# Performance work log

Hardware: AMD Instinct MI355X
Metric: run time of the kernel (lower is better)

## Reference

```python
import jax, jax.numpy as jnp
import numpy as np

N_HEADS = 16
EPS = 1e-6

def _feature_map(x):
    return jax.nn.elu(x) + 1.0

def setup_inputs() -> dict:
    key = jax.random.key(0)
    k1, k2, k3 = jax.random.split(key, 3)
    B, S, D = 1, 2048, 1024
    x = jax.random.normal(k1, (B, S, D), dtype=jnp.float32)
    causal_mask = jnp.tril(jnp.ones((S, S), dtype=bool))[None, None]  # (1,1,S,S)
    # scale weights like nn.Linear default init (roughly 1/sqrt(fan_in))
    W_qkv = jax.random.normal(k2, (D, 3 * D), dtype=jnp.float32) / np.sqrt(D)
    W_out = jax.random.normal(k3, (D, D), dtype=jnp.float32) / np.sqrt(D)
    return {"x": x, "causal_mask": causal_mask, "W_qkv": W_qkv, "W_out": W_out}

def reference(x, causal_mask, W_qkv, W_out):
    B, S, D = x.shape
    H = N_HEADS
    hd = D // H
    qkv = x @ W_qkv                              # (B,S,3D)
    q, k, v = jnp.split(qkv, 3, axis=-1)
    def to_heads(t):
        return t.reshape(B, S, H, hd).transpose(0, 2, 1, 3)  # (B,H,S,hd)
    q, k, v = to_heads(q), to_heads(k), to_heads(v)
    phi_q = _feature_map(q)
    phi_k = _feature_map(k)
    k_cum = jnp.cumsum(phi_k, axis=2)                        # (B,H,S,hd)
    kv = jnp.einsum('bhsi,bhsj->bhsij', phi_k, v)            # (B,H,S,hd,hd)
    kv_cum = jnp.cumsum(kv, axis=2)
    numer = jnp.einsum('bhsi,bhsij->bhsj', phi_q, kv_cum)    # (B,H,S,hd)
    denom = jnp.einsum('bhsi,bhsi->bhs', phi_q, k_cum) + EPS
    attn_out = numer / denom[..., None]
    attn_out = attn_out.transpose(0, 2, 1, 3).reshape(B, S, D)
    return attn_out @ W_out
```

## Files before the change

kernel.cpp:

```cpp
#include <hip/hip_runtime.h>
#include <cstddef>
#include <cstdint>

#define SEQ 2048
#define DIM 1024
#define NH 16
#define HD 64
#define CK 64
#define NCK (SEQ / CK)
#define KVR 65
#define KVRP 80

typedef __attribute__((ext_vector_type(8))) short short8;
typedef __attribute__((ext_vector_type(8))) unsigned short ushort8;
typedef __attribute__((ext_vector_type(4))) float fx4;

__device__ __forceinline__ float phi_fn(float x) {
    return x > 0.f ? x + 1.f : __expf(x);
}
__device__ __forceinline__ float bf2f(unsigned short u) {
    return __uint_as_float((unsigned int)u << 16);
}
__device__ __forceinline__ unsigned short f2bf(float f) {
    unsigned int u = __float_as_uint(f);
    unsigned int r = (u + 0x7FFFu + ((u >> 16) & 1u)) >> 16;
    return (unsigned short)r;
}

__device__ __forceinline__ void lds_write16(unsigned short* base, int row, int col, short8 v) {
    int byte = row * 128 + col * 2; byte ^= (row & 7) << 4;
    *(short8*)((char*)base + byte) = v;
}
__device__ __forceinline__ void lds_write2(unsigned short* base, int row, int col, unsigned short v) {
    int byte = row * 128 + col * 2; byte ^= (row & 7) << 4;
    *(unsigned short*)((char*)base + byte) = v;
}
__device__ __forceinline__ short8 lds_read_frag(const unsigned short* base, int row, int kcol) {
    int byte = row * 128 + kcol * 2; byte ^= (row & 7) << 4;
    return *(const short8*)((const char*)base + byte);
}

template<int N> __device__ __forceinline__ void waitv() {
    if constexpr (N == 0)       asm volatile("s_waitcnt vmcnt(0)"  ::: "memory");
    else if constexpr (N == 4)  asm volatile("s_waitcnt vmcnt(4)"  ::: "memory");
    else if constexpr (N == 5)  asm volatile("s_waitcnt vmcnt(5)"  ::: "memory");
    else if constexpr (N == 6)  asm volatile("s_waitcnt vmcnt(6)"  ::: "memory");
    else if constexpr (N == 8)  asm volatile("s_waitcnt vmcnt(8)"  ::: "memory");
    else if constexpr (N == 10) asm volatile("s_waitcnt vmcnt(10)" ::: "memory");
    else if constexpr (N == 12) asm volatile("s_waitcnt vmcnt(12)" ::: "memory");
    else                        asm volatile("s_waitcnt vmcnt(0)"  ::: "memory");
}

__global__ __launch_bounds__(256)
void to_bf16_vec(const float* __restrict__ in, unsigned short* __restrict__ out, int n)
{
    const int i = (blockIdx.x * 256 + threadIdx.x) * 4;
    if (i >= n) return;
    float4 v = *(const float4*)&in[i];
    ushort4 o;
    o.x = f2bf(v.x); o.y = f2bf(v.y); o.z = f2bf(v.z); o.w = f2bf(v.w);
    *(ushort4*)&out[i] = o;
}

__global__ __launch_bounds__(256)
void transpose2_to_bf16(const float* __restrict__ W1, unsigned short* __restrict__ WT1,
                        const float* __restrict__ W2, unsigned short* __restrict__ WT2)
{
    __shared__ float t[32][33];
    const float* W; unsigned short* WT; int N, kb, nb;
    if (blockIdx.x < 96 * 32) {
        W = W1; WT = WT1; N = 3 * DIM;
        nb = (blockIdx.x % 96) * 32; kb = (blockIdx.x / 96) * 32;
    } else {
        const int b = blockIdx.x - 96 * 32;
        W = W2; WT = WT2; N = DIM;
        nb = (b % 32) * 32; kb = (b / 32) * 32;
    }
    const int c = threadIdx.x & 31, r0 = threadIdx.x >> 5;
    #pragma unroll
    for (int i = 0; i < 4; ++i) {
        const int r = r0 + i * 8;
        t[r][c] = W[(size_t)(kb + r) * N + nb + c];
    }
    __syncthreads();
    #pragma unroll
    for (int i = 0; i < 4; ++i) {
        const int r = r0 + i * 8;
        WT[(size_t)(nb + r) * DIM + kb + c] = f2bf(t[c][r]);
    }
}

template<int WAVES_M, int WAVES_N, int NFRAG, int OUT_BF16>
__global__ __launch_bounds__(WAVES_M * WAVES_N * 64)
void gemm_pipe(const unsigned short* __restrict__ A,
               const unsigned short* __restrict__ BT,
               void* __restrict__ Cout, int M, int N, int K)
{
    constexpr int BN      = WAVES_N * NFRAG * 16;
    constexpr int THREADS = WAVES_M * WAVES_N * 64;
    constexpr int CHUNK   = THREADS * 16;
    constexpr int ALOADS  = (128 * 64 * 2) / CHUNK;
    constexpr int BLOADS  = (BN * 64 * 2) / CHUNK;
    constexpr int LOADS   = ALOADS + BLOADS;

    __shared__ unsigned short As[3][128 * 64];
    __shared__ unsigned short Bs[3][BN * 64];

    const int tid = threadIdx.x, lane = tid & 63, wave = tid >> 6;
    const int wm = (wave / WAVES_N) * 64;
    const int wn = (wave % WAVES_N) * (NFRAG * 16);

    int wg = blockIdx.y * gridDim.x + blockIdx.x;
    const int cpx = (gridDim.x * gridDim.y) >> 3;
    wg = (wg & 7) * cpx + (wg >> 3);
    const int bx = wg / gridDim.y;
    const int by = wg % gridDim.y;

    const int m0 = by * 128, n0 = bx * BN;
    const unsigned short* Abase = A + (size_t)m0 * K;
    const unsigned short* Bbase = BT + (size_t)n0 * K;
    const int nt = K >> 6;
    const int fr = lane & 15, fk = (lane >> 4) * 8;

    fx4 acc[4][NFRAG] = {};

    auto STAGE = [&](int slot, int t) {
        const int k0 = t << 6;
        #pragma unroll
        for (int q = 0; q < ALOADS; ++q) {
            const int L = q * CHUNK + tid * 16;
            const int row = L >> 7;
            const int srcb = L ^ ((row & 7) << 4);
            const unsigned short* g = Abase + (size_t)row * K + k0 + ((srcb & 127) >> 1);
            __builtin_amdgcn_global_load_lds(
                (const __attribute__((address_space(1))) void*)g,
                (__attribute__((address_space(3))) void*)((char*)&As[slot][0] + q * CHUNK + wave * 1024),
                16, 0, 0);
        }
        #pragma unroll
        for (int q = 0; q < BLOADS; ++q) {
            const int L = q * CHUNK + tid * 16;
            const int row = L >> 7;
            const int srcb = L ^ ((row & 7) << 4);
            const unsigned short* g = Bbase + (size_t)row * K + k0 + ((srcb & 127) >> 1);
            __builtin_amdgcn_global_load_lds(
                (const __attribute__((address_space(1))) void*)g,
                (__attribute__((address_space(3))) void*)((char*)&Bs[slot][0] + q * CHUNK + wave * 1024),
                16, 0, 0);
        }
    };

    STAGE(0, 0); STAGE(1, 1); STAGE(2, 2);
    waitv<2 * LOADS>();
    __builtin_amdgcn_s_barrier();

    int cur = 0;
    for (int t = 0; t < nt; ++t) {
        short8 a0[4], a1[4], b0[NFRAG], b1[NFRAG];
        #pragma unroll
        for (int i = 0; i < 4; ++i) {
            a0[i] = lds_read_frag(&As[cur][0], wm + i * 16 + fr, fk);
            a1[i] = lds_read_frag(&As[cur][0], wm + i * 16 + fr, 32 + fk);
        }
        #pragma unroll
        for (int j = 0; j < NFRAG; ++j) {
            b0[j] = lds_read_frag(&Bs[cur][0], wn + j * 16 + fr, fk);
            b1[j] = lds_read_frag(&Bs[cur][0], wn + j * 16 + fr, 32 + fk);
        }
        asm volatile("s_waitcnt lgkmcnt(0)" ::: "memory");
        __builtin_amdgcn_sched_barrier(0);
        __builtin_amdgcn_s_barrier();

        const bool refill = (t + 3 < nt);
        if (refill) STAGE(cur, t + 3);

        __builtin_amdgcn_s_setprio(1);
        #pragma unroll
        for (int i = 0; i < 4; ++i)
            #pragma unroll
            for (int j = 0; j < NFRAG; ++j)
                acc[i][j] = __builtin_amdgcn_mfma_f32_16x16x32_bf16(a0[i], b0[j], acc[i][j], 0, 0, 0);
        #pragma unroll
        for (int i = 0; i < 4; ++i)
            #pragma unroll
            for (int j = 0; j < NFRAG; ++j)
                acc[i][j] = __builtin_amdgcn_mfma_f32_16x16x32_bf16(a1[i], b1[j], acc[i][j], 0, 0, 0);
        __builtin_amdgcn_s_setprio(0);

        if (refill)            waitv<2 * LOADS>();
        else if (t == nt - 3)  waitv<LOADS>();
        else                   waitv<0>();
        __builtin_amdgcn_s_barrier();
        cur = (cur == 2) ? 0 : cur + 1;
    }

    const int cr = (lane >> 4) * 4, cc = lane & 15;
    #pragma unroll
    for (int i = 0; i < 4; ++i)
        #pragma unroll
        for (int j = 0; j < NFRAG; ++j) {
            const int m = m0 + wm + i * 16 + cr;
            const int n = n0 + wn + j * 16 + cc;
            #pragma unroll
            for (int r = 0; r < 4; ++r) {
                const float v = acc[i][j][r];
                if (OUT_BF16)
                    ((unsigned short*)Cout)[(size_t)(m + r) * N + n] = f2bf(v);
                else
                    ((float*)Cout)[(size_t)(m + r) * N + n] = v;
            }
        }
}

__global__ __launch_bounds__(256)
void chunk_kv(const unsigned short* __restrict__ qkv, float* __restrict__ kvs)
{
    const int c = blockIdx.x, h = blockIdx.y;
    __shared__ unsigned short kT[64 * 64];
    __shared__ unsigned short vT[KVRP * 64];
    const int tid = threadIdx.x, lane = tid & 63, wave = tid >> 6;
    const int s0 = c * CK;

    #pragma unroll
    for (int part = 0; part < 2; ++part) {
        const int s = (tid >> 3) + part * 32;
        const int d0 = (tid & 7) * 8;
        const size_t base = (size_t)(s0 + s) * (3 * DIM) + (size_t)h * HD + d0;
        ushort8 kk = *(const ushort8*)&qkv[base + DIM];
        ushort8 vv = *(const ushort8*)&qkv[base + 2 * DIM];
        #pragma unroll
        for (int u = 0; u < 8; ++u) {
            lds_write2(kT, d0 + u, s, f2bf(phi_fn(bf2f(kk[u]))));
            lds_write2(vT, d0 + u, s, vv[u]);
        }
    }
    if (tid < 64) lds_write2(vT, 64, tid, 0x3F80);
    for (int idx = tid; idx < 15 * 64; idx += 256)
        lds_write2(vT, 65 + (idx >> 6), idx & 63, 0);
    __syncthreads();

    fx4 acc[5] = {};
    #pragma unroll
    for (int ks = 0; ks < 2; ++ks) {
        short8 b = lds_read_frag(kT, wave * 16 + (lane & 15), ks * 32 + (lane >> 4) * 8);
        #pragma unroll
        for (int mt = 0; mt < 5; ++mt) {
            short8 a = lds_read_frag(vT, mt * 16 + (lane & 15), ks * 32 + (lane >> 4) * 8);
            acc[mt] = __builtin_amdgcn_mfma_f32_16x16x32_bf16(a, b, acc[mt], 0, 0, 0);
        }
    }
    float* dst = kvs + (size_t)(h * NCK + c) * KVR * 64;
    const int i = wave * 16 + (lane & 15);
    #pragma unroll
    for (int mt = 0; mt < 5; ++mt)
        #pragma unroll
        for (int t = 0; t < 4; ++t) {
            const int j = mt * 16 + (lane >> 4) * 4 + t;
            if (j < KVR) dst[(size_t)j * 64 + i] = acc[mt][t];
        }
}

__global__ __launch_bounds__(256)
void scan_kv(const float* __restrict__ kvs, unsigned short* __restrict__ kvpb)
{
    const int e = blockIdx.x * 256 + threadIdx.x;
    if (e >= NH * KVR * 64) return;
    const int h = e / (KVR * 64), off = e % (KVR * 64);
    const float* src = kvs + (size_t)h * NCK * KVR * 64 + off;
    unsigned short* dst = kvpb + (size_t)h * NCK * KVR * 64 + off;
    float v[NCK];
    #pragma unroll
    for (int c2 = 0; c2 < NCK; ++c2) v[c2] = src[(size_t)c2 * KVR * 64];
    float run = 0.f;
    #pragma unroll
    for (int c2 = 0; c2 < NCK; ++c2) {
        dst[(size_t)c2 * KVR * 64] = f2bf(run);
        run += v[c2];
    }
}

__global__ __launch_bounds__(256)
void attn_chunk(const unsigned short* __restrict__ qkv,
                const unsigned short* __restrict__ kvpb,
                unsigned short* __restrict__ attnb)
{
    const int c = blockIdx.x, h = blockIdx.y;
    __shared__ unsigned short q_s[64 * 64];
    __shared__ unsigned short k_s[64 * 64];
    __shared__ unsigned short p_s[64 * 64];
    __shared__ unsigned short vT[KVRP * 64];
    __shared__ unsigned short kvp[KVRP * 64];
    const int tid = threadIdx.x, lane = tid & 63, wave = tid >> 6;
    const int s0 = c * CK;

    #pragma unroll
    for (int part = 0; part < 2; ++part) {
        const int s = (tid >> 3) + part * 32;
        const int d0 = (tid & 7) * 8;
        const size_t base = (size_t)(s0 + s) * (3 * DIM) + (size_t)h * HD + d0;
        ushort8 qq = *(const ushort8*)&qkv[base];
        ushort8 kk = *(const ushort8*)&qkv[base + DIM];
        ushort8 vv = *(const ushort8*)&qkv[base + 2 * DIM];
        short8 qo, ko;
        #pragma unroll
        for (int u = 0; u < 8; ++u) {
            qo[u] = (short)f2bf(phi_fn(bf2f(qq[u])));
            ko[u] = (short)f2bf(phi_fn(bf2f(kk[u])));
        }
        lds_write16(q_s, s, d0, qo);
        lds_write16(k_s, s, d0, ko);
        #pragma unroll
        for (int u = 0; u < 8; ++u)
            lds_write2(vT, d0 + u, s, vv[u]);
    }
    const unsigned short* kv_src = kvpb + (size_t)(h * NCK + c) * KVR * 64;
    for (int idx = tid * 8; idx < KVR * 64; idx += 2048) {
        ushort8 kv8 = *(const ushort8*)&kv_src[idx];
        short8 kv8s;
        #pragma unroll
        for (int u = 0; u < 8; ++u) kv8s[u] = (short)kv8[u];
        lds_write16(kvp, idx >> 6, idx & 63, kv8s);
    }
    if (tid < 64) lds_write2(vT, 64, tid, 0x3F80);
    for (int idx = tid; idx < 15 * 64; idx += 256) {
        lds_write2(vT, 65 + (idx >> 6), idx & 63, 0);
        lds_write2(kvp, 65 + (idx >> 6), idx & 63, 0);
    }
    __syncthreads();

    const int r0 = wave * 16;
    fx4 accp[4] = {};
    #pragma unroll
    for (int ks = 0; ks < 2; ++ks) {
        short8 aq = lds_read_frag(q_s, r0 + (lane & 15), ks * 32 + (lane >> 4) * 8);
        #pragma unroll
        for (int nt = 0; nt < 4; ++nt) {
            short8 bk = lds_read_frag(k_s, nt * 16 + (lane & 15), ks * 32 + (lane >> 4) * 8);
            accp[nt] = __builtin_amdgcn_mfma_f32_16x16x32_bf16(aq, bk, accp[nt], 0, 0, 0);
        }
    }
    #pragma unroll
    for (int nt = 0; nt < 4; ++nt)
        #pragma unroll
        for (int t = 0; t < 4; ++t) {
            const int r = r0 + (lane >> 4) * 4 + t, sc = nt * 16 + (lane & 15);
            lds_write2(p_s, r, sc, (sc <= r) ? f2bf(accp[nt][t]) : (unsigned short)0);
        }
    __syncthreads();

    fx4 acc[5] = {};
    #pragma unroll
    for (int ks = 0; ks < 2; ++ks) {
        short8 ap = lds_read_frag(p_s, r0 + (lane & 15), ks * 32 + (lane >> 4) * 8);
        short8 aq = lds_read_frag(q_s, r0 + (lane & 15), ks * 32 + (lane >> 4) * 8);
        #pragma unroll
        for (int nt = 0; nt < 5; ++nt) {
            short8 bv  = lds_read_frag(vT,  nt * 16 + (lane & 15), ks * 32 + (lane >> 4) * 8);
            short8 bkv = lds_read_frag(kvp, nt * 16 + (lane & 15), ks * 32 + (lane >> 4) * 8);
            acc[nt] = __builtin_amdgcn_mfma_f32_16x16x32_bf16(ap, bv,  acc[nt], 0, 0, 0);
            acc[nt] = __builtin_amdgcn_mfma_f32_16x16x32_bf16(aq, bkv, acc[nt], 0, 0, 0);
        }
    }
    float dinv[4];
    #pragma unroll
    for (int t = 0; t < 4; ++t) {
        const float d = __shfl(acc[4][t], lane & 48, 64);
        dinv[t] = 1.f / (d + 1e-6f);
    }
    #pragma unroll
    for (int nt = 0; nt < 4; ++nt)
        #pragma unroll
        for (int t = 0; t < 4; ++t) {
            const int r = r0 + (lane >> 4) * 4 + t, j = nt * 16 + (lane & 15);
            attnb[(size_t)(s0 + r) * DIM + (size_t)h * HD + j] = f2bf(acc[nt][t] * dinv[t]);
        }
}

extern "C" void kernel_launch(void* const* d_in, const int* in_sizes, int n_in,
                              void* d_out, int out_size, void* d_ws, size_t ws_size,
                              hipStream_t stream)
{
    const float* x     = (const float*)d_in[0];
    const float* W_qkv = (const float*)d_in[2];
    const float* W_out = (const float*)d_in[3];
    float* out = (float*)d_out;

    char* ws = (char*)d_ws;
    size_t off = 0;
    unsigned short* qkvb = (unsigned short*)(ws + off); off += (size_t)SEQ * 3 * DIM * 2;
    unsigned short* xb   = (unsigned short*)(ws + off); off += (size_t)SEQ * DIM * 2;
    float*          kvs  = (float*)         (ws + off); off += (size_t)NH * NCK * KVR * 64 * 4;
    unsigned short* kvpb = (unsigned short*)(ws + off); off += (size_t)NH * NCK * KVR * 64 * 2;
    unsigned short* wqt  = (unsigned short*)(ws + off); off += (size_t)3 * DIM * DIM * 2;
    unsigned short* wot  = (unsigned short*)(ws + off); off += (size_t)DIM * DIM * 2;
    unsigned short* attnb = xb;

    dim3 blk(256);

    to_bf16_vec<<<dim3(SEQ * DIM / 1024), blk, 0, stream>>>(x, xb, SEQ * DIM);
    transpose2_to_bf16<<<dim3(96 * 32 + 32 * 32), blk, 0, stream>>>(W_qkv, wqt, W_out, wot);

    gemm_pipe<2, 4, 3, 1><<<dim3(3 * DIM / 192, SEQ / 128), dim3(512), 0, stream>>>(
        xb, wqt, qkvb, SEQ, 3 * DIM, DIM);

    chunk_kv<<<dim3(NCK, NH), blk, 0, stream>>>(qkvb, kvs);
    scan_kv<<<dim3((NH * KVR * 64 + 255) / 256), blk, 0, stream>>>(kvs, kvpb);
    attn_chunk<<<dim3(NCK, NH), blk, 0, stream>>>(qkvb, kvpb, attnb);

    gemm_pipe<2, 2, 2, 0><<<dim3(DIM / 64, SEQ / 128), dim3(256), 0, stream>>>(
        attnb, wot, out, SEQ, DIM, DIM);
}
```

Baseline: 66.40 us.

## Fuse prep kernels and restructure GEMM pipeline to prefetch two stages ahead

Merges the x-to-bf16 conversion and the weight transpose kernels into one launch, removing one kernel launch and its tail. The GEMM main loop now keeps two stages in flight instead of three. It issues the next stage's async loads after the LDS fragment reads and before the MFMAs, which drops one barrier per iteration. Prefetch depth is shallower, so there is less latency hiding for the global-to-LDS loads.

```diff
diff --git a/kernel.cpp b/kernel.cpp
--- a/kernel.cpp
+++ b/kernel.cpp
@@ -52,27 +52,27 @@
 }
 
 __global__ __launch_bounds__(256)
-void to_bf16_vec(const float* __restrict__ in, unsigned short* __restrict__ out, int n)
-{
-    const int i = (blockIdx.x * 256 + threadIdx.x) * 4;
-    if (i >= n) return;
-    float4 v = *(const float4*)&in[i];
-    ushort4 o;
-    o.x = f2bf(v.x); o.y = f2bf(v.y); o.z = f2bf(v.z); o.w = f2bf(v.w);
-    *(ushort4*)&out[i] = o;
-}
-
-__global__ __launch_bounds__(256)
-void transpose2_to_bf16(const float* __restrict__ W1, unsigned short* __restrict__ WT1,
-                        const float* __restrict__ W2, unsigned short* __restrict__ WT2)
+void prep_fused(const float* __restrict__ x, unsigned short* __restrict__ xb,
+                const float* __restrict__ W1, unsigned short* __restrict__ WT1,
+                const float* __restrict__ W2, unsigned short* __restrict__ WT2)
 {
     __shared__ float t[32][33];
+    int b = blockIdx.x;
+    if (b < 2048) {
+        const int i = (b * 256 + threadIdx.x) * 4;
+        float4 v = *(const float4*)&x[i];
+        ushort4 o;
+        o.x = f2bf(v.x); o.y = f2bf(v.y); o.z = f2bf(v.z); o.w = f2bf(v.w);
+        *(ushort4*)&xb[i] = o;
+        return;
+    }
+    b -= 2048;
     const float* W; unsigned short* WT; int N, kb, nb;
-    if (blockIdx.x < 96 * 32) {
+    if (b < 96 * 32) {
         W = W1; WT = WT1; N = 3 * DIM;
-        nb = (blockIdx.x % 96) * 32; kb = (blockIdx.x / 96) * 32;
+        nb = (b % 96) * 32; kb = (b / 96) * 32;
     } else {
-        const int b = blockIdx.x - 96 * 32;
+        b -= 96 * 32;
         W = W2; WT = WT2; N = DIM;
         nb = (b % 32) * 32; kb = (b / 32) * 32;
     }
@@ -150,12 +150,12 @@
         }
     };
 
-    STAGE(0, 0); STAGE(1, 1); STAGE(2, 2);
-    waitv<2 * LOADS>();
+    STAGE(0, 0); STAGE(1, 1);
+    waitv<LOADS>();
     __builtin_amdgcn_s_barrier();
 
-    int cur = 0;
     for (int t = 0; t < nt; ++t) {
+        const int cur = t % 3;
         short8 a0[4], a1[4], b0[NFRAG], b1[NFRAG];
         #pragma unroll
         for (int i = 0; i < 4; ++i) {
@@ -167,12 +167,12 @@
             b0[j] = lds_read_frag(&Bs[cur][0], wn + j * 16 + fr, fk);
             b1[j] = lds_read_frag(&Bs[cur][0], wn + j * 16 + fr, 32 + fk);
         }
+
+        const bool pf = (t + 2 < nt);
+        if (pf) STAGE((t + 2) % 3, t + 2);
+
         asm volatile("s_waitcnt lgkmcnt(0)" ::: "memory");
         __builtin_amdgcn_sched_barrier(0);
-        __builtin_amdgcn_s_barrier();
-
-        const bool refill = (t + 3 < nt);
-        if (refill) STAGE(cur, t + 3);
 
         __builtin_amdgcn_s_setprio(1);
         #pragma unroll
@@ -187,11 +187,8 @@
                 acc[i][j] = __builtin_amdgcn_mfma_f32_16x16x32_bf16(a1[i], b1[j], acc[i][j], 0, 0, 0);
         __builtin_amdgcn_s_setprio(0);
 
-        if (refill)            waitv<2 * LOADS>();
-        else if (t == nt - 3)  waitv<LOADS>();
-        else                   waitv<0>();
+        if (pf) waitv<LOADS>(); else waitv<0>();
         __builtin_amdgcn_s_barrier();
-        cur = (cur == 2) ? 0 : cur + 1;
     }
 
     const int cr = (lane >> 4) * 4, cc = lane & 15;
@@ -397,8 +394,8 @@
 
     dim3 blk(256);
 
-    to_bf16_vec<<<dim3(SEQ * DIM / 1024), blk, 0, stream>>>(x, xb, SEQ * DIM);
-    transpose2_to_bf16<<<dim3(96 * 32 + 32 * 32), blk, 0, stream>>>(W_qkv, wqt, W_out, wot);
+    prep_fused<<<dim3(2048 + 96 * 32 + 32 * 32), blk, 0, stream>>>(
+        x, xb, W_qkv, wqt, W_out, wot);
 
     gemm_pipe<2, 4, 3, 1><<<dim3(3 * DIM / 192, SEQ / 128), dim3(512), 0, stream>>>(
         xb, wqt, qkvb, SEQ, 3 * DIM, DIM);
```

After: 58.74 us. -11.5%, faster.
